# Kernel optimization log

Measured on AMD Instinct MI355X. Metric: run time of the kernel, lower is better.

Reference implementation:

```python
import jax, jax.numpy as jnp
import numpy as np

N_NODES = 100000
IN_CH = 128
HID = 16
N_EDGES = 3200000


def setup_inputs() -> dict:
    key = jax.random.key(0)
    k1, k2, k3, k4 = jax.random.split(key, 4)
    x = jax.random.normal(k1, (N_NODES, IN_CH), dtype=jnp.float32)
    edge_index = jax.random.randint(k2, (2, N_EDGES), 0, N_NODES, dtype=jnp.int64)
    s1 = 1.0 / np.sqrt(IN_CH)
    s2 = 1.0 / np.sqrt(HID)
    W1 = jax.random.uniform(k3, (IN_CH, HID), dtype=jnp.float32, minval=-s1, maxval=s1)
    b1 = jnp.zeros((HID,), dtype=jnp.float32)
    W2 = jax.random.uniform(k4, (HID, HID), dtype=jnp.float32, minval=-s2, maxval=s2)
    b2 = jnp.zeros((HID,), dtype=jnp.float32)
    return {"x": x, "edge_index": edge_index, "W1": W1, "b1": b1, "W2": W2, "b2": b2}


def _gcn_layer(h, W, b, row, col, norm, n_nodes):
    # GCNConv: transform first (small hidden dim), then normalized sum aggregation
    h = h @ W  # [N, out]
    msg = h[row] * norm[:, None]  # gather over edges incl. self-loops
    out = jax.ops.segment_sum(msg, col, num_segments=n_nodes)
    return out + b


def reference(x, edge_index, W1, b1, W2, b2):
    n = x.shape[0]
    row, col = edge_index[0], edge_index[1]
    # add self-loops (PyG GCNConv default)
    loop = jnp.arange(n, dtype=edge_index.dtype)
    row_l = jnp.concatenate([row, loop])
    col_l = jnp.concatenate([col, loop])
    # symmetric normalization D^-1/2 (A+I) D^-1/2 (degree from target index)
    deg = jax.ops.segment_sum(jnp.ones_like(col_l, dtype=x.dtype), col_l, num_segments=n)
    dinv = jnp.where(deg > 0, jax.lax.rsqrt(deg), 0.0)
    norm = dinv[row_l] * dinv[col_l]

    h = _gcn_layer(x, W1, b1, row_l, col_l, norm, n)
    h = jax.nn.relu(h)  # dropout is identity at eval
    h = _gcn_layer(h, W2, b2, row_l, col_l, norm, n)

    # fused per-edge dot-product link score + sigmoid (original edges only)
    scores = jnp.sum(h[row] * h[col], axis=-1)
    return jax.nn.sigmoid(scores)
```

## Files before the change

### kernel.cpp

```cpp
#include <hip/hip_runtime.h>
#include <hip/hip_bf16.h>
#include <hip/hip_fp16.h>
#include <math.h>


#define BSH 9
#define BSZ 512
#define MAXCH 3200
#define MAXCHUNKS 1024

__global__ __launch_bounds__(512) void pA(const int* __restrict__ col,
                                          int* __restrict__ M, int E, int CH, int NBUK) {
    __shared__ int hist[256];
    const int t = threadIdx.x, b = blockIdx.x;
    if (t < 256) hist[t] = 0;
    __syncthreads();
    const int s = b * CH, e = min(E, s + CH);
    const int n4 = (e - s) >> 2;
    const int4* c4 = (const int4*)(col + s);
    for (int i = t; i < n4; i += 512) {
        int4 c = c4[i];
        atomicAdd(&hist[c.x >> BSH], 1);
        atomicAdd(&hist[c.y >> BSH], 1);
        atomicAdd(&hist[c.z >> BSH], 1);
        atomicAdd(&hist[c.w >> BSH], 1);
    }
    for (int i = s + (n4 << 2) + t; i < e; i += 512) atomicAdd(&hist[col[i] >> BSH], 1);
    __syncthreads();
    for (int i = t; i < NBUK; i += 512) M[b * NBUK + i] = hist[i];
}

__global__ __launch_bounds__(1024) void pB1(int* __restrict__ M, int* __restrict__ T,
                                            int NBUK, int CN) {
    __shared__ int s[1024];
    const int t = threadIdx.x, k = blockIdx.x;
    int own = (t < CN) ? M[t * NBUK + k] : 0;
    s[t] = own;
    __syncthreads();
    for (int d = 1; d < 1024; d <<= 1) {
        int add = (t >= d) ? s[t - d] : 0;
        __syncthreads();
        s[t] += add;
        __syncthreads();
    }
    if (t < CN) M[t * NBUK + k] = s[t] - own;
    if (t == 1023) T[k] = s[1023];
}

__global__ __launch_bounds__(512) void pB2(const int* __restrict__ T, int* __restrict__ S,
                                           int* __restrict__ start, int NBUK, int N, int E) {
    __shared__ int s[512];
    const int t = threadIdx.x;
    int own = (t < NBUK) ? T[t] : 0;
    s[t] = own;
    __syncthreads();
    for (int d = 1; d < 512; d <<= 1) {
        int add = (t >= d) ? s[t - d] : 0;
        __syncthreads();
        s[t] += add;
        __syncthreads();
    }
    if (t < NBUK) S[t] = s[t] - own;
    if (t == 511) S[NBUK] = s[511];
    if (t == 0) start[N] = E;
}

__global__ __launch_bounds__(512) void pC(const int* __restrict__ row, const int* __restrict__ col,
                                          const int* __restrict__ M, const int* __restrict__ S,
                                          unsigned int* __restrict__ ebuf, int E, int CH, int NBUK) {
    __shared__ unsigned int se[MAXCH];
    __shared__ unsigned short pk[MAXCH];
    __shared__ int lhist[256], lbase[256], lcur[256], gbase[256];
    const int t = threadIdx.x, b = blockIdx.x;
    if (t < 256) lhist[t] = 0;
    __syncthreads();
    const int s = b * CH, e = min(E, s + CH);
    const int cnt = e - s;
    const int n4 = cnt >> 2;
    const int4* c4 = (const int4*)(col + s);
    const int4* r4 = (const int4*)(row + s);
    for (int i = t; i < n4; i += 512) {
        int4 c = c4[i];
        atomicAdd(&lhist[c.x >> BSH], 1);
        atomicAdd(&lhist[c.y >> BSH], 1);
        atomicAdd(&lhist[c.z >> BSH], 1);
        atomicAdd(&lhist[c.w >> BSH], 1);
    }
    for (int i = (n4 << 2) + t; i < cnt; i += 512) atomicAdd(&lhist[col[s + i] >> BSH], 1);
    __syncthreads();
    {
        int own = (t < 256) ? lhist[t] : 0;
        if (t < 256) lcur[t] = own;
        __syncthreads();
        for (int d = 1; d < 256; d <<= 1) {
            int add = (t < 256 && t >= d) ? lcur[t - d] : 0;
            __syncthreads();
            if (t < 256) lcur[t] += add;
            __syncthreads();
        }
        if (t < 256) {
            lbase[t] = lcur[t] - own;
            lcur[t] = lcur[t] - own;
        }
        __syncthreads();
        if (t < NBUK) gbase[t] = S[t] + M[b * NBUK + t] - lbase[t];
    }
    __syncthreads();
    for (int i = t; i < n4; i += 512) {
        int4 c = c4[i];
        int4 r = r4[i];
        int k0 = c.x >> BSH, p0 = atomicAdd(&lcur[k0], 1);
        se[p0] = ((unsigned int)(c.x & (BSZ - 1)) << 17) | (unsigned int)r.x; pk[p0] = (unsigned short)k0;
        int k1 = c.y >> BSH, p1 = atomicAdd(&lcur[k1], 1);
        se[p1] = ((unsigned int)(c.y & (BSZ - 1)) << 17) | (unsigned int)r.y; pk[p1] = (unsigned short)k1;
        int k2 = c.z >> BSH, p2 = atomicAdd(&lcur[k2], 1);
        se[p2] = ((unsigned int)(c.z & (BSZ - 1)) << 17) | (unsigned int)r.z; pk[p2] = (unsigned short)k2;
        int k3 = c.w >> BSH, p3 = atomicAdd(&lcur[k3], 1);
        se[p3] = ((unsigned int)(c.w & (BSZ - 1)) << 17) | (unsigned int)r.w; pk[p3] = (unsigned short)k3;
    }
    for (int i = (n4 << 2) + t; i < cnt; i += 512) {
        int c = col[s + i], r = row[s + i];
        int k = c >> BSH, p = atomicAdd(&lcur[k], 1);
        se[p] = ((unsigned int)(c & (BSZ - 1)) << 17) | (unsigned int)r; pk[p] = (unsigned short)k;
    }
    __syncthreads();
    for (int i = t; i < cnt; i += 512) {
        int k = pk[i];
        ebuf[gbase[k] + i] = se[i];
    }
}

__global__ __launch_bounds__(1024) void pC2(const unsigned int* __restrict__ ebuf,
                                            const int* __restrict__ S,
                                            unsigned int* __restrict__ ebuf2,
                                            float* __restrict__ dinv,
                                            int* __restrict__ start, int N) {
    __shared__ int h[BSZ], sc[BSZ], cur[BSZ];
    const int t = threadIdx.x, k = blockIdx.x;
    if (t < BSZ) h[t] = 0;
    __syncthreads();
    const int s = S[k], e = S[k + 1];
    for (int i = s + t; i < e; i += 1024) atomicAdd(&h[ebuf[i] >> 17], 1);
    __syncthreads();
    if (t < BSZ) sc[t] = h[t];
    __syncthreads();
    for (int d = 1; d < BSZ; d <<= 1) {
        int add = (t < BSZ && t >= d) ? sc[t - d] : 0;
        __syncthreads();
        if (t < BSZ) sc[t] += add;
        __syncthreads();
    }
    if (t < BSZ) {
        cur[t] = sc[t] - h[t];
        const int v = (k << BSH) + t;
        if (v < N) {
            dinv[v] = rsqrtf((float)h[t] + 1.0f);
            start[v] = s + cur[t];
        }
    }
    __syncthreads();
    for (int i = s + t; i < e; i += 1024) {
        unsigned int w = ebuf[i];
        int p = atomicAdd(&cur[w >> 17], 1);
        ebuf2[s + p] = w;
    }
}

__global__ __launch_bounds__(256) void k_gemm1(
    const float* __restrict__ x, const float* __restrict__ W1,
    const float* __restrict__ dinv, __half* __restrict__ ts, int N) {
    __shared__ float wsT[16 * 132];
    const int tid = threadIdx.x;
    for (int idx = tid; idx < 2048; idx += 256) {
        int k = idx >> 4, c = idx & 15;
        wsT[c * 132 + k] = W1[idx];
    }
    __syncthreads();
    const int n = blockIdx.x * 256 + tid;
    if (n >= N) return;
    const float4* xr = (const float4*)(x + (size_t)n * 128);
    float acc[16];
    #pragma unroll
    for (int c = 0; c < 16; ++c) acc[c] = 0.f;
    #pragma unroll 4
    for (int k4 = 0; k4 < 32; ++k4) {
        float4 a = xr[k4];
        #pragma unroll
        for (int c = 0; c < 16; ++c) {
            const float4 w = *(const float4*)&wsT[c * 132 + k4 * 4];
            acc[c] = fmaf(a.x, w.x, fmaf(a.y, w.y, fmaf(a.z, w.z, fmaf(a.w, w.w, acc[c]))));
        }
    }
    float dv = dinv[n];
    union { __half h[16]; uint4 u[2]; } o;
    #pragma unroll
    for (int c = 0; c < 16; ++c) o.h[c] = __float2half(acc[c] * dv);
    uint4* dst = (uint4*)(ts + (size_t)n * 16);
    dst[0] = o.u[0]; dst[1] = o.u[1];
}

__global__ __launch_bounds__(256) void pGat1(
    const unsigned int* __restrict__ ebuf2, const int* __restrict__ start,
    const __half2* __restrict__ tsv, const float* __restrict__ dinv,
    const float* __restrict__ b1, const float* __restrict__ W2,
    __half2* __restrict__ ts2v, int N) {
    __shared__ float w2s[256];
    const int tid = threadIdx.x;
    w2s[tid] = W2[tid];
    __syncthreads();
    const int l = tid & 7;
    const int v = blockIdx.x * 32 + (tid >> 3);
    if (v >= N) return;
    const int s = start[v], e = start[v + 1];
    float sx = 0.f, sy = 0.f;
    int i = s;
    for (; i + 8 <= e; i += 8) {
        unsigned int w0 = ebuf2[i],     w1 = ebuf2[i + 1];
        unsigned int w2 = ebuf2[i + 2], w3 = ebuf2[i + 3];
        unsigned int w4 = ebuf2[i + 4], w5 = ebuf2[i + 5];
        unsigned int w6 = ebuf2[i + 6], w7 = ebuf2[i + 7];
        float2 f0 = __half22float2(tsv[(size_t)(w0 & 0x1FFFF) * 8 + l]);
        float2 f1 = __half22float2(tsv[(size_t)(w1 & 0x1FFFF) * 8 + l]);
        float2 f2 = __half22float2(tsv[(size_t)(w2 & 0x1FFFF) * 8 + l]);
        float2 f3 = __half22float2(tsv[(size_t)(w3 & 0x1FFFF) * 8 + l]);
        float2 f4 = __half22float2(tsv[(size_t)(w4 & 0x1FFFF) * 8 + l]);
        float2 f5 = __half22float2(tsv[(size_t)(w5 & 0x1FFFF) * 8 + l]);
        float2 f6 = __half22float2(tsv[(size_t)(w6 & 0x1FFFF) * 8 + l]);
        float2 f7 = __half22float2(tsv[(size_t)(w7 & 0x1FFFF) * 8 + l]);
        sx += ((f0.x + f1.x) + (f2.x + f3.x)) + ((f4.x + f5.x) + (f6.x + f7.x));
        sy += ((f0.y + f1.y) + (f2.y + f3.y)) + ((f4.y + f5.y) + (f6.y + f7.y));
    }
    for (; i + 4 <= e; i += 4) {
        unsigned int w0 = ebuf2[i],     w1 = ebuf2[i + 1];
        unsigned int w2 = ebuf2[i + 2], w3 = ebuf2[i + 3];
        float2 f0 = __half22float2(tsv[(size_t)(w0 & 0x1FFFF) * 8 + l]);
        float2 f1 = __half22float2(tsv[(size_t)(w1 & 0x1FFFF) * 8 + l]);
        float2 f2 = __half22float2(tsv[(size_t)(w2 & 0x1FFFF) * 8 + l]);
        float2 f3 = __half22float2(tsv[(size_t)(w3 & 0x1FFFF) * 8 + l]);
        sx += (f0.x + f1.x) + (f2.x + f3.x);
        sy += (f0.y + f1.y) + (f2.y + f3.y);
    }
    for (; i < e; ++i) {
        unsigned int w = ebuf2[i];
        float2 f = __half22float2(tsv[(size_t)(w & 0x1FFFF) * 8 + l]);
        sx += f.x; sy += f.y;
    }
    const float dv = dinv[v];
    float2 sf = __half22float2(tsv[(size_t)v * 8 + l]);
    float hx = fmaxf(dv * (sx + sf.x) + b1[2 * l],     0.f);
    float hy = fmaxf(dv * (sy + sf.y) + b1[2 * l + 1], 0.f);
    float ox = 0.f, oy = 0.f;
    #pragma unroll
    for (int j = 0; j < 8; ++j) {
        float ax = __shfl(hx, j, 8);
        float ay = __shfl(hy, j, 8);
        ox = fmaf(ax, w2s[(2 * j) * 16 + 2 * l],     fmaf(ay, w2s[(2 * j + 1) * 16 + 2 * l],     ox));
        oy = fmaf(ax, w2s[(2 * j) * 16 + 2 * l + 1], fmaf(ay, w2s[(2 * j + 1) * 16 + 2 * l + 1], oy));
    }
    ts2v[(size_t)v * 8 + l] = __halves2half2(__float2half(dv * ox), __float2half(dv * oy));
}

__global__ __launch_bounds__(256) void pGat2(
    const unsigned int* __restrict__ ebuf2, const int* __restrict__ start,
    const __half2* __restrict__ tsv, const float* __restrict__ dinv,
    const float* __restrict__ b2, __half2* __restrict__ h2v, int N) {
    const int tid = threadIdx.x;
    const int l = tid & 7;
    const int v = blockIdx.x * 32 + (tid >> 3);
    if (v >= N) return;
    const int s = start[v], e = start[v + 1];
    float sx = 0.f, sy = 0.f;
    int i = s;
    for (; i + 8 <= e; i += 8) {
        unsigned int w0 = ebuf2[i],     w1 = ebuf2[i + 1];
        unsigned int w2 = ebuf2[i + 2], w3 = ebuf2[i + 3];
        unsigned int w4 = ebuf2[i + 4], w5 = ebuf2[i + 5];
        unsigned int w6 = ebuf2[i + 6], w7 = ebuf2[i + 7];
        float2 f0 = __half22float2(tsv[(size_t)(w0 & 0x1FFFF) * 8 + l]);
        float2 f1 = __half22float2(tsv[(size_t)(w1 & 0x1FFFF) * 8 + l]);
        float2 f2 = __half22float2(tsv[(size_t)(w2 & 0x1FFFF) * 8 + l]);
        float2 f3 = __half22float2(tsv[(size_t)(w3 & 0x1FFFF) * 8 + l]);
        float2 f4 = __half22float2(tsv[(size_t)(w4 & 0x1FFFF) * 8 + l]);
        float2 f5 = __half22float2(tsv[(size_t)(w5 & 0x1FFFF) * 8 + l]);
        float2 f6 = __half22float2(tsv[(size_t)(w6 & 0x1FFFF) * 8 + l]);
        float2 f7 = __half22float2(tsv[(size_t)(w7 & 0x1FFFF) * 8 + l]);
        sx += ((f0.x + f1.x) + (f2.x + f3.x)) + ((f4.x + f5.x) + (f6.x + f7.x));
        sy += ((f0.y + f1.y) + (f2.y + f3.y)) + ((f4.y + f5.y) + (f6.y + f7.y));
    }
    for (; i + 4 <= e; i += 4) {
        unsigned int w0 = ebuf2[i],     w1 = ebuf2[i + 1];
        unsigned int w2 = ebuf2[i + 2], w3 = ebuf2[i + 3];
        float2 f0 = __half22float2(tsv[(size_t)(w0 & 0x1FFFF) * 8 + l]);
        float2 f1 = __half22float2(tsv[(size_t)(w1 & 0x1FFFF) * 8 + l]);
        float2 f2 = __half22float2(tsv[(size_t)(w2 & 0x1FFFF) * 8 + l]);
        float2 f3 = __half22float2(tsv[(size_t)(w3 & 0x1FFFF) * 8 + l]);
        sx += (f0.x + f1.x) + (f2.x + f3.x);
        sy += (f0.y + f1.y) + (f2.y + f3.y);
    }
    for (; i < e; ++i) {
        unsigned int w = ebuf2[i];
        float2 f = __half22float2(tsv[(size_t)(w & 0x1FFFF) * 8 + l]);
        sx += f.x; sy += f.y;
    }
    float2 sf = __half22float2(tsv[(size_t)v * 8 + l]);
    const float dv = dinv[v];
    h2v[(size_t)v * 8 + l] = __halves2half2(
        __float2half(dv * (sx + sf.x) + b2[2 * l]),
        __float2half(dv * (sy + sf.y) + b2[2 * l + 1]));
}

__global__ void k_score(const int* __restrict__ row, const int* __restrict__ col,
                        const __half* __restrict__ h2h, float* __restrict__ out, int E) {
    int e = blockIdx.x * 256 + threadIdx.x;
    if (e < E) {
        union { uint4 u[2]; __half2 h[8]; } a, b;
        const uint4* pa = (const uint4*)(h2h + (size_t)row[e] * 16);
        const uint4* pb = (const uint4*)(h2h + (size_t)col[e] * 16);
        a.u[0] = pa[0]; a.u[1] = pa[1];
        b.u[0] = pb[0]; b.u[1] = pb[1];
        float d = 0.f;
        #pragma unroll
        for (int i = 0; i < 8; ++i) {
            float2 fa = __half22float2(a.h[i]);
            float2 fb = __half22float2(b.h[i]);
            d = fmaf(fa.x, fb.x, fmaf(fa.y, fb.y, d));
        }
        out[e] = 1.0f / (1.0f + __expf(-d));
    }
}

__global__ void k_countf(const int* __restrict__ col, float* __restrict__ deg, int E) {
    int e = blockIdx.x * 256 + threadIdx.x;
    if (e < E) atomicAdd(&deg[col[e]], 1.0f);
}
__global__ void k_dinvf(float* __restrict__ dinv, int N) {
    int v = blockIdx.x * 256 + threadIdx.x;
    if (v < N) dinv[v] = rsqrtf(dinv[v] + 1.0f);
}
__global__ __launch_bounds__(256) void k_gemm1f(
    const float* __restrict__ x, const float* __restrict__ W1,
    const float* __restrict__ dinv, float* __restrict__ ts, int N) {
    __shared__ float wsT[16 * 132];
    const int tid = threadIdx.x;
    for (int idx = tid; idx < 2048; idx += 256) {
        int k = idx >> 4, c = idx & 15;
        wsT[c * 132 + k] = W1[idx];
    }
    __syncthreads();
    const int n = blockIdx.x * 256 + tid;
    if (n >= N) return;
    const float4* xr = (const float4*)(x + (size_t)n * 128);
    float acc[16];
    #pragma unroll
    for (int c = 0; c < 16; ++c) acc[c] = 0.f;
    for (int k4 = 0; k4 < 32; ++k4) {
        float4 a = xr[k4];
        #pragma unroll
        for (int c = 0; c < 16; ++c) {
            const float4 w = *(const float4*)&wsT[c * 132 + k4 * 4];
            acc[c] = fmaf(a.x, w.x, fmaf(a.y, w.y, fmaf(a.z, w.z, fmaf(a.w, w.w, acc[c]))));
        }
    }
    float dv = dinv[n];
    float4* o = (float4*)(ts + (size_t)n * 16);
    #pragma unroll
    for (int q = 0; q < 4; ++q)
        o[q] = make_float4(acc[4*q] * dv, acc[4*q+1] * dv, acc[4*q+2] * dv, acc[4*q+3] * dv);
}
__global__ void k_scatter(const int* __restrict__ row, const int* __restrict__ col,
                          const float* __restrict__ ts, float* __restrict__ acc, int E) {
    int g = blockIdx.x * 256 + threadIdx.x;
    int e = g >> 4, c = g & 15;
    if (e < E) atomicAdd(&acc[(size_t)col[e] * 16 + c], ts[(size_t)row[e] * 16 + c]);
}
__global__ void k_finalize(float* __restrict__ acc, const float* __restrict__ ts,
                           const float* __restrict__ dinv, const float* __restrict__ b,
                           int N, int relu) {
    int g = blockIdx.x * 256 + threadIdx.x;
    int v = g >> 4, c = g & 15;
    if (v < N) {
        float h = dinv[v] * (acc[g] + ts[g]) + b[c];
        if (relu) h = fmaxf(h, 0.f);
        acc[g] = h;
    }
}
__global__ __launch_bounds__(256) void k_gemm2f(
    const float* __restrict__ h1, const float* __restrict__ W2,
    const float* __restrict__ dinv, float* __restrict__ ts2, int N) {
    __shared__ float hs[16 * 17];
    __shared__ float ws2[256];
    const int tid = threadIdx.x;
    const int base = blockIdx.x * 16;
    if (tid < 64) ((float4*)ws2)[tid] = ((const float4*)W2)[tid];
    if (tid >= 64 && tid < 128) {
        int t2 = tid - 64;
        float4 v4 = ((const float4*)(h1 + (size_t)base * 16))[t2];
        float* d = &hs[(t2 >> 2) * 17 + (t2 & 3) * 4];
        d[0] = v4.x; d[1] = v4.y; d[2] = v4.z; d[3] = v4.w;
    }
    __syncthreads();
    const int r = tid >> 4, c = tid & 15;
    float a = 0.f;
    #pragma unroll
    for (int kk = 0; kk < 16; ++kk) a = fmaf(hs[r * 17 + kk], ws2[kk * 16 + c], a);
    ts2[(size_t)(base + r) * 16 + c] = a * dinv[base + r];
}
__global__ void k_scoref(const int* __restrict__ row, const int* __restrict__ col,
                         const float* __restrict__ h2, float* __restrict__ out, int E) {
    int e = blockIdx.x * 256 + threadIdx.x;
    if (e < E) {
        const float4* a = (const float4*)(h2 + (size_t)row[e] * 16);
        const float4* b = (const float4*)(h2 + (size_t)col[e] * 16);
        float d = 0.f;
        #pragma unroll
        for (int i = 0; i < 4; ++i) {
            float4 u = a[i], v = b[i];
            d += u.x * v.x + u.y * v.y + u.z * v.z + u.w * v.w;
        }
        out[e] = 1.0f / (1.0f + __expf(-d));
    }
}

extern "C" void kernel_launch(void* const* d_in, const int* in_sizes, int n_in,
                              void* d_out, int out_size, void* d_ws, size_t ws_size,
                              hipStream_t stream) {
    const float* x  = (const float*)d_in[0];
    const int*   ei = (const int*)d_in[1];
    const float* W1 = (const float*)d_in[2];
    const float* b1 = (const float*)d_in[3];
    const float* W2 = (const float*)d_in[4];
    const float* b2 = (const float*)d_in[5];

    const int N = in_sizes[0] / 128;
    const int E = in_sizes[1] / 2;
    const int* row = ei;
    const int* col = ei + E;
    float* out = (float*)d_out;

    const int NBUK = (N + BSZ - 1) / BSZ;
    const int CN = (E + MAXCH - 1) / MAXCH;
    const int CH = MAXCH;

    char* ws = (char*)d_ws;
    size_t off = 0;
    auto alloc = [&](size_t bytes) { void* p = ws + off; off += (bytes + 255) & ~(size_t)255; return p; };
    float*  dinv  = (float*)alloc((size_t)N * 4);
    __half* ts1h  = (__half*)alloc((size_t)N * 32);
    __half* ts2h  = (__half*)alloc((size_t)N * 32);
    int*    start = (int*)alloc((size_t)(N + 1) * 4);
    int*    M     = (int*)alloc((size_t)CN * NBUK * 4);
    int*    T     = (int*)alloc((size_t)NBUK * 4);
    int*    S     = (int*)alloc((size_t)(NBUK + 1) * 4);
    unsigned int* ebuf  = (unsigned int*)alloc((size_t)E * 4);
    unsigned int* ebuf2 = (unsigned int*)alloc((size_t)E * 4);
    const size_t need = off;

    if (N <= 131072 && NBUK <= 256 && CN <= MAXCHUNKS && ws_size >= need) {
        pA <<<CN, 512, 0, stream>>>(col, M, E, CH, NBUK);
        pB1<<<NBUK, 1024, 0, stream>>>(M, T, NBUK, CN);
        pB2<<<1, 512, 0, stream>>>(T, S, start, NBUK, N, E);
        pC <<<CN, 512, 0, stream>>>(row, col, M, S, ebuf, E, CH, NBUK);
        pC2<<<NBUK, 1024, 0, stream>>>(ebuf, S, ebuf2, dinv, start, N);
        k_gemm1<<<(N + 255) / 256, 256, 0, stream>>>(x, W1, dinv, ts1h, N);
        pGat1<<<(N + 31) / 32, 256, 0, stream>>>(ebuf2, start, (const __half2*)ts1h, dinv, b1, W2,
                                                 (__half2*)ts2h, N);
        __half* h2h = ts1h;
        pGat2<<<(N + 31) / 32, 256, 0, stream>>>(ebuf2, start, (const __half2*)ts2h, dinv, b2,
                                                 (__half2*)h2h, N);
        k_score<<<(E + 255) / 256, 256, 0, stream>>>(row, col, h2h, out, E);
    } else {
        float* dinvF = (float*)ws;
        float* ts1F  = (float*)(ws + (size_t)N * 4);
        float* ts2F  = (float*)(ws + (size_t)N * 4 + (size_t)N * 64);
        hipMemsetAsync(dinvF, 0, (size_t)N * 4, stream);
        hipMemsetAsync(ts2F, 0, (size_t)N * 64, stream);
        k_countf<<<(E + 255) / 256, 256, 0, stream>>>(col, dinvF, E);
        k_dinvf<<<(N + 255) / 256, 256, 0, stream>>>(dinvF, N);
        k_gemm1f<<<(N + 255) / 256, 256, 0, stream>>>(x, W1, dinvF, ts1F, N);
        k_scatter<<<(E * 16) / 256, 256, 0, stream>>>(row, col, ts1F, ts2F, E);
        k_finalize<<<(N * 16 + 255) / 256, 256, 0, stream>>>(ts2F, ts1F, dinvF, b1, N, 1);
        k_gemm2f<<<N / 16, 256, 0, stream>>>(ts2F, W2, dinvF, ts1F, N);
        hipMemsetAsync(ts2F, 0, (size_t)N * 64, stream);
        k_scatter<<<(E * 16) / 256, 256, 0, stream>>>(row, col, ts1F, ts2F, E);
        k_finalize<<<(N * 16 + 255) / 256, 256, 0, stream>>>(ts2F, ts1F, dinvF, b2, N, 0);
        k_scoref<<<(E + 255) / 256, 256, 0, stream>>>(row, col, ts2F, out, E);
    }
}
```

Before: 253.9 us.

## Fuse per-bucket local sort into gather kernels and compute degrees via global atomics

Shrinks destination buckets to 128 nodes and drops the separate pC2 second-level sort pass and its ebuf2 buffer. Each gather kernel now re-sorts its bucket's edges in shared memory before aggregating, and falls back to a slow scan when a bucket exceeds capacity. Degrees are counted with global atomics in pA, and dinv is computed inside gemm1. This removes one full pass over the edge list and a buffer, but the local sort is done twice and pA now issues millions of global atomics.

```diff
diff --git a/kernel.cpp b/kernel.cpp
--- a/kernel.cpp
+++ b/kernel.cpp
@@ -4,28 +4,34 @@
 #include <math.h>
 
 
-#define BSH 9
-#define BSZ 512
+#define BSH 7
+#define BSZ 128
+#define CAP 8192
 #define MAXCH 3200
 #define MAXCHUNKS 1024
 
 __global__ __launch_bounds__(512) void pA(const int* __restrict__ col,
-                                          int* __restrict__ M, int E, int CH, int NBUK) {
-    __shared__ int hist[256];
+                                          int* __restrict__ M, int* __restrict__ degi,
+                                          int E, int CH, int NBUK) {
+    __shared__ int hist[1024];
     const int t = threadIdx.x, b = blockIdx.x;
-    if (t < 256) hist[t] = 0;
+    for (int i = t; i < 1024; i += 512) hist[i] = 0;
     __syncthreads();
     const int s = b * CH, e = min(E, s + CH);
     const int n4 = (e - s) >> 2;
     const int4* c4 = (const int4*)(col + s);
     for (int i = t; i < n4; i += 512) {
         int4 c = c4[i];
-        atomicAdd(&hist[c.x >> BSH], 1);
-        atomicAdd(&hist[c.y >> BSH], 1);
-        atomicAdd(&hist[c.z >> BSH], 1);
-        atomicAdd(&hist[c.w >> BSH], 1);
-    }
-    for (int i = s + (n4 << 2) + t; i < e; i += 512) atomicAdd(&hist[col[i] >> BSH], 1);
+        atomicAdd(&hist[c.x >> BSH], 1); atomicAdd(&degi[c.x], 1);
+        atomicAdd(&hist[c.y >> BSH], 1); atomicAdd(&degi[c.y], 1);
+        atomicAdd(&hist[c.z >> BSH], 1); atomicAdd(&degi[c.z], 1);
+        atomicAdd(&hist[c.w >> BSH], 1); atomicAdd(&degi[c.w], 1);
+    }
+    for (int i = s + (n4 << 2) + t; i < e; i += 512) {
+        int c = col[i];
+        atomicAdd(&hist[c >> BSH], 1);
+        atomicAdd(&degi[c], 1);
+    }
     __syncthreads();
     for (int i = t; i < NBUK; i += 512) M[b * NBUK + i] = hist[i];
 }
@@ -47,66 +53,63 @@
     if (t == 1023) T[k] = s[1023];
 }
 
-__global__ __launch_bounds__(512) void pB2(const int* __restrict__ T, int* __restrict__ S,
-                                           int* __restrict__ start, int NBUK, int N, int E) {
-    __shared__ int s[512];
+__global__ __launch_bounds__(1024) void pB2(const int* __restrict__ T, int* __restrict__ S,
+                                            int NBUK) {
+    __shared__ int s[1024];
     const int t = threadIdx.x;
     int own = (t < NBUK) ? T[t] : 0;
     s[t] = own;
     __syncthreads();
-    for (int d = 1; d < 512; d <<= 1) {
+    for (int d = 1; d < 1024; d <<= 1) {
         int add = (t >= d) ? s[t - d] : 0;
         __syncthreads();
         s[t] += add;
         __syncthreads();
     }
     if (t < NBUK) S[t] = s[t] - own;
-    if (t == 511) S[NBUK] = s[511];
-    if (t == 0) start[N] = E;
-}
-
-__global__ __launch_bounds__(512) void pC(const int* __restrict__ row, const int* __restrict__ col,
-                                          const int* __restrict__ M, const int* __restrict__ S,
-                                          unsigned int* __restrict__ ebuf, int E, int CH, int NBUK) {
+    if (t == 1023) S[NBUK] = s[1023];
+}
+
+__global__ __launch_bounds__(1024) void pC(const int* __restrict__ row, const int* __restrict__ col,
+                                           const int* __restrict__ M, const int* __restrict__ S,
+                                           unsigned int* __restrict__ ebuf, int E, int CH, int NBUK) {
     __shared__ unsigned int se[MAXCH];
     __shared__ unsigned short pk[MAXCH];
-    __shared__ int lhist[256], lbase[256], lcur[256], gbase[256];
+    __shared__ int lhist[1024], lbase[1024], lcur[1024], gbase[1024];
     const int t = threadIdx.x, b = blockIdx.x;
-    if (t < 256) lhist[t] = 0;
+    lhist[t] = 0;
     __syncthreads();
     const int s = b * CH, e = min(E, s + CH);
     const int cnt = e - s;
     const int n4 = cnt >> 2;
     const int4* c4 = (const int4*)(col + s);
     const int4* r4 = (const int4*)(row + s);
-    for (int i = t; i < n4; i += 512) {
+    for (int i = t; i < n4; i += 1024) {
         int4 c = c4[i];
         atomicAdd(&lhist[c.x >> BSH], 1);
         atomicAdd(&lhist[c.y >> BSH], 1);
         atomicAdd(&lhist[c.z >> BSH], 1);
         atomicAdd(&lhist[c.w >> BSH], 1);
     }
-    for (int i = (n4 << 2) + t; i < cnt; i += 512) atomicAdd(&lhist[col[s + i] >> BSH], 1);
+    for (int i = (n4 << 2) + t; i < cnt; i += 1024) atomicAdd(&lhist[col[s + i] >> BSH], 1);
     __syncthreads();
     {
-        int own = (t < 256) ? lhist[t] : 0;
-        if (t < 256) lcur[t] = own;
-        __syncthreads();
-        for (int d = 1; d < 256; d <<= 1) {
-            int add = (t < 256 && t >= d) ? lcur[t - d] : 0;
+        int own = lhist[t];
+        lcur[t] = own;
+        __syncthreads();
+        for (int d = 1; d < 1024; d <<= 1) {
+            int add = (t >= d) ? lcur[t - d] : 0;
             __syncthreads();
-            if (t < 256) lcur[t] += add;
+            lcur[t] += add;
             __syncthreads();
         }
-        if (t < 256) {
-            lbase[t] = lcur[t] - own;
-            lcur[t] = lcur[t] - own;
-        }
+        lbase[t] = lcur[t] - own;
+        lcur[t] = lbase[t];
         __syncthreads();
         if (t < NBUK) gbase[t] = S[t] + M[b * NBUK + t] - lbase[t];
     }
     __syncthreads();
-    for (int i = t; i < n4; i += 512) {
+    for (int i = t; i < n4; i += 1024) {
         int4 c = c4[i];
         int4 r = r4[i];
         int k0 = c.x >> BSH, p0 = atomicAdd(&lcur[k0], 1);
@@ -118,57 +121,22 @@
         int k3 = c.w >> BSH, p3 = atomicAdd(&lcur[k3], 1);
         se[p3] = ((unsigned int)(c.w & (BSZ - 1)) << 17) | (unsigned int)r.w; pk[p3] = (unsigned short)k3;
     }
-    for (int i = (n4 << 2) + t; i < cnt; i += 512) {
+    for (int i = (n4 << 2) + t; i < cnt; i += 1024) {
         int c = col[s + i], r = row[s + i];
         int k = c >> BSH, p = atomicAdd(&lcur[k], 1);
         se[p] = ((unsigned int)(c & (BSZ - 1)) << 17) | (unsigned int)r; pk[p] = (unsigned short)k;
     }
     __syncthreads();
-    for (int i = t; i < cnt; i += 512) {
+    for (int i = t; i < cnt; i += 1024) {
         int k = pk[i];
         ebuf[gbase[k] + i] = se[i];
     }
 }
 
-__global__ __launch_bounds__(1024) void pC2(const unsigned int* __restrict__ ebuf,
-                                            const int* __restrict__ S,
-                                            unsigned int* __restrict__ ebuf2,
-                                            float* __restrict__ dinv,
-                                            int* __restrict__ start, int N) {
-    __shared__ int h[BSZ], sc[BSZ], cur[BSZ];
-    const int t = threadIdx.x, k = blockIdx.x;
-    if (t < BSZ) h[t] = 0;
-    __syncthreads();
-    const int s = S[k], e = S[k + 1];
-    for (int i = s + t; i < e; i += 1024) atomicAdd(&h[ebuf[i] >> 17], 1);
-    __syncthreads();
-    if (t < BSZ) sc[t] = h[t];
-    __syncthreads();
-    for (int d = 1; d < BSZ; d <<= 1) {
-        int add = (t < BSZ && t >= d) ? sc[t - d] : 0;
-        __syncthreads();
-        if (t < BSZ) sc[t] += add;
-        __syncthreads();
-    }
-    if (t < BSZ) {
-        cur[t] = sc[t] - h[t];
-        const int v = (k << BSH) + t;
-        if (v < N) {
-            dinv[v] = rsqrtf((float)h[t] + 1.0f);
-            start[v] = s + cur[t];
-        }
-    }
-    __syncthreads();
-    for (int i = s + t; i < e; i += 1024) {
-        unsigned int w = ebuf[i];
-        int p = atomicAdd(&cur[w >> 17], 1);
-        ebuf2[s + p] = w;
-    }
-}
-
 __global__ __launch_bounds__(256) void k_gemm1(
     const float* __restrict__ x, const float* __restrict__ W1,
-    const float* __restrict__ dinv, __half* __restrict__ ts, int N) {
+    const int* __restrict__ degi, float* __restrict__ dinv,
+    __half* __restrict__ ts, int N) {
     __shared__ float wsT[16 * 132];
     const int tid = threadIdx.x;
     for (int idx = tid; idx < 2048; idx += 256) {
@@ -191,7 +159,8 @@
             acc[c] = fmaf(a.x, w.x, fmaf(a.y, w.y, fmaf(a.z, w.z, fmaf(a.w, w.w, acc[c]))));
         }
     }
-    float dv = dinv[n];
+    const float dv = rsqrtf((float)degi[n] + 1.0f);
+    dinv[n] = dv;
     union { __half h[16]; uint4 u[2]; } o;
     #pragma unroll
     for (int c = 0; c < 16; ++c) o.h[c] = __float2half(acc[c] * dv);
@@ -199,114 +168,159 @@
     dst[0] = o.u[0]; dst[1] = o.u[1];
 }
 
-__global__ __launch_bounds__(256) void pGat1(
-    const unsigned int* __restrict__ ebuf2, const int* __restrict__ start,
+__global__ __launch_bounds__(512) void pG1(
+    const unsigned int* __restrict__ ebuf, const int* __restrict__ S,
     const __half2* __restrict__ tsv, const float* __restrict__ dinv,
     const float* __restrict__ b1, const float* __restrict__ W2,
     __half2* __restrict__ ts2v, int N) {
+    __shared__ unsigned int se[CAP];
+    __shared__ int h[BSZ], sc[BSZ], cur[BSZ];
     __shared__ float w2s[256];
-    const int tid = threadIdx.x;
-    w2s[tid] = W2[tid];
-    __syncthreads();
-    const int l = tid & 7;
-    const int v = blockIdx.x * 32 + (tid >> 3);
-    if (v >= N) return;
-    const int s = start[v], e = start[v + 1];
-    float sx = 0.f, sy = 0.f;
-    int i = s;
-    for (; i + 8 <= e; i += 8) {
-        unsigned int w0 = ebuf2[i],     w1 = ebuf2[i + 1];
-        unsigned int w2 = ebuf2[i + 2], w3 = ebuf2[i + 3];
-        unsigned int w4 = ebuf2[i + 4], w5 = ebuf2[i + 5];
-        unsigned int w6 = ebuf2[i + 6], w7 = ebuf2[i + 7];
-        float2 f0 = __half22float2(tsv[(size_t)(w0 & 0x1FFFF) * 8 + l]);
-        float2 f1 = __half22float2(tsv[(size_t)(w1 & 0x1FFFF) * 8 + l]);
-        float2 f2 = __half22float2(tsv[(size_t)(w2 & 0x1FFFF) * 8 + l]);
-        float2 f3 = __half22float2(tsv[(size_t)(w3 & 0x1FFFF) * 8 + l]);
-        float2 f4 = __half22float2(tsv[(size_t)(w4 & 0x1FFFF) * 8 + l]);
-        float2 f5 = __half22float2(tsv[(size_t)(w5 & 0x1FFFF) * 8 + l]);
-        float2 f6 = __half22float2(tsv[(size_t)(w6 & 0x1FFFF) * 8 + l]);
-        float2 f7 = __half22float2(tsv[(size_t)(w7 & 0x1FFFF) * 8 + l]);
-        sx += ((f0.x + f1.x) + (f2.x + f3.x)) + ((f4.x + f5.x) + (f6.x + f7.x));
-        sy += ((f0.y + f1.y) + (f2.y + f3.y)) + ((f4.y + f5.y) + (f6.y + f7.y));
-    }
-    for (; i + 4 <= e; i += 4) {
-        unsigned int w0 = ebuf2[i],     w1 = ebuf2[i + 1];
-        unsigned int w2 = ebuf2[i + 2], w3 = ebuf2[i + 3];
-        float2 f0 = __half22float2(tsv[(size_t)(w0 & 0x1FFFF) * 8 + l]);
-        float2 f1 = __half22float2(tsv[(size_t)(w1 & 0x1FFFF) * 8 + l]);
-        float2 f2 = __half22float2(tsv[(size_t)(w2 & 0x1FFFF) * 8 + l]);
-        float2 f3 = __half22float2(tsv[(size_t)(w3 & 0x1FFFF) * 8 + l]);
-        sx += (f0.x + f1.x) + (f2.x + f3.x);
-        sy += (f0.y + f1.y) + (f2.y + f3.y);
-    }
-    for (; i < e; ++i) {
-        unsigned int w = ebuf2[i];
-        float2 f = __half22float2(tsv[(size_t)(w & 0x1FFFF) * 8 + l]);
-        sx += f.x; sy += f.y;
-    }
-    const float dv = dinv[v];
-    float2 sf = __half22float2(tsv[(size_t)v * 8 + l]);
-    float hx = fmaxf(dv * (sx + sf.x) + b1[2 * l],     0.f);
-    float hy = fmaxf(dv * (sy + sf.y) + b1[2 * l + 1], 0.f);
-    float ox = 0.f, oy = 0.f;
-    #pragma unroll
-    for (int j = 0; j < 8; ++j) {
-        float ax = __shfl(hx, j, 8);
-        float ay = __shfl(hy, j, 8);
-        ox = fmaf(ax, w2s[(2 * j) * 16 + 2 * l],     fmaf(ay, w2s[(2 * j + 1) * 16 + 2 * l],     ox));
-        oy = fmaf(ax, w2s[(2 * j) * 16 + 2 * l + 1], fmaf(ay, w2s[(2 * j + 1) * 16 + 2 * l + 1], oy));
-    }
-    ts2v[(size_t)v * 8 + l] = __halves2half2(__float2half(dv * ox), __float2half(dv * oy));
-}
-
-__global__ __launch_bounds__(256) void pGat2(
-    const unsigned int* __restrict__ ebuf2, const int* __restrict__ start,
+    const int t = threadIdx.x, k = blockIdx.x;
+    if (t < BSZ) h[t] = 0;
+    if (t < 256) w2s[t] = W2[t];
+    __syncthreads();
+    const int s = S[k], e = S[k + 1];
+    const int cnt = e - s;
+    if (cnt <= CAP) {
+        for (int i = s + t; i < e; i += 512) atomicAdd(&h[ebuf[i] >> 17], 1);
+        __syncthreads();
+        if (t < BSZ) sc[t] = h[t];
+        __syncthreads();
+        for (int d = 1; d < BSZ; d <<= 1) {
+            int add = (t < BSZ && t >= d) ? sc[t - d] : 0;
+            __syncthreads();
+            if (t < BSZ) sc[t] += add;
+            __syncthreads();
+        }
+        if (t < BSZ) cur[t] = sc[t] - h[t];
+        __syncthreads();
+        for (int i = s + t; i < e; i += 512) {
+            unsigned int w = ebuf[i];
+            int p = atomicAdd(&cur[w >> 17], 1);
+            se[p] = w;
+        }
+        __syncthreads();
+    }
+    const int l = t & 7;
+    #pragma unroll
+    for (int sweep = 0; sweep < 2; ++sweep) {
+        const int lv = (t >> 3) + (sweep << 6);
+        const int v = (k << BSH) + lv;
+        if (v >= N) continue;
+        float sx = 0.f, sy = 0.f;
+        if (cnt <= CAP) {
+            const int pe = sc[lv];
+            int i = pe - h[lv];
+            for (; i + 4 <= pe; i += 4) {
+                unsigned int w0 = se[i], w1 = se[i + 1], w2 = se[i + 2], w3 = se[i + 3];
+                float2 f0 = __half22float2(tsv[(size_t)(w0 & 0x1FFFF) * 8 + l]);
+                float2 f1 = __half22float2(tsv[(size_t)(w1 & 0x1FFFF) * 8 + l]);
+                float2 f2 = __half22float2(tsv[(size_t)(w2 & 0x1FFFF) * 8 + l]);
+                float2 f3 = __half22float2(tsv[(size_t)(w3 & 0x1FFFF) * 8 + l]);
+                sx += (f0.x + f1.x) + (f2.x + f3.x);
+                sy += (f0.y + f1.y) + (f2.y + f3.y);
+            }
+            for (; i < pe; ++i) {
+                unsigned int w = se[i];
+                float2 f = __half22float2(tsv[(size_t)(w & 0x1FFFF) * 8 + l]);
+                sx += f.x; sy += f.y;
+            }
+        } else {
+            for (int j = s; j < e; ++j) {
+                unsigned int w = ebuf[j];
+                if ((int)(w >> 17) == lv) {
+                    float2 f = __half22float2(tsv[(size_t)(w & 0x1FFFF) * 8 + l]);
+                    sx += f.x; sy += f.y;
+                }
+            }
+        }
+        const float dv = dinv[v];
+        float2 sf = __half22float2(tsv[(size_t)v * 8 + l]);
+        float hx = fmaxf(dv * (sx + sf.x) + b1[2 * l],     0.f);
+        float hy = fmaxf(dv * (sy + sf.y) + b1[2 * l + 1], 0.f);
+        float ox = 0.f, oy = 0.f;
+        #pragma unroll
+        for (int j = 0; j < 8; ++j) {
+            float ax = __shfl(hx, j, 8);
+            float ay = __shfl(hy, j, 8);
+            ox = fmaf(ax, w2s[(2 * j) * 16 + 2 * l],     fmaf(ay, w2s[(2 * j + 1) * 16 + 2 * l],     ox));
+            oy = fmaf(ax, w2s[(2 * j) * 16 + 2 * l + 1], fmaf(ay, w2s[(2 * j + 1) * 16 + 2 * l + 1], oy));
+        }
+        ts2v[(size_t)v * 8 + l] = __halves2half2(__float2half(dv * ox), __float2half(dv * oy));
+    }
+}
+
+__global__ __launch_bounds__(512) void pG2(
+    const unsigned int* __restrict__ ebuf, const int* __restrict__ S,
     const __half2* __restrict__ tsv, const float* __restrict__ dinv,
     const float* __restrict__ b2, __half2* __restrict__ h2v, int N) {
-    const int tid = threadIdx.x;
-    const int l = tid & 7;
-    const int v = blockIdx.x * 32 + (tid >> 3);
-    if (v >= N) return;
-    const int s = start[v], e = start[v + 1];
-    float sx = 0.f, sy = 0.f;
-    int i = s;
-    for (; i + 8 <= e; i += 8) {
-        unsigned int w0 = ebuf2[i],     w1 = ebuf2[i + 1];
-        unsigned int w2 = ebuf2[i + 2], w3 = ebuf2[i + 3];
-        unsigned int w4 = ebuf2[i + 4], w5 = ebuf2[i + 5];
-        unsigned int w6 = ebuf2[i + 6], w7 = ebuf2[i + 7];
-        float2 f0 = __half22float2(tsv[(size_t)(w0 & 0x1FFFF) * 8 + l]);
-        float2 f1 = __half22float2(tsv[(size_t)(w1 & 0x1FFFF) * 8 + l]);
-        float2 f2 = __half22float2(tsv[(size_t)(w2 & 0x1FFFF) * 8 + l]);
-        float2 f3 = __half22float2(tsv[(size_t)(w3 & 0x1FFFF) * 8 + l]);
-        float2 f4 = __half22float2(tsv[(size_t)(w4 & 0x1FFFF) * 8 + l]);
-        float2 f5 = __half22float2(tsv[(size_t)(w5 & 0x1FFFF) * 8 + l]);
-        float2 f6 = __half22float2(tsv[(size_t)(w6 & 0x1FFFF) * 8 + l]);
-        float2 f7 = __half22float2(tsv[(size_t)(w7 & 0x1FFFF) * 8 + l]);
-        sx += ((f0.x + f1.x) + (f2.x + f3.x)) + ((f4.x + f5.x) + (f6.x + f7.x));
-        sy += ((f0.y + f1.y) + (f2.y + f3.y)) + ((f4.y + f5.y) + (f6.y + f7.y));
-    }
-    for (; i + 4 <= e; i += 4) {
-        unsigned int w0 = ebuf2[i],     w1 = ebuf2[i + 1];
-        unsigned int w2 = ebuf2[i + 2], w3 = ebuf2[i + 3];
-        float2 f0 = __half22float2(tsv[(size_t)(w0 & 0x1FFFF) * 8 + l]);
-        float2 f1 = __half22float2(tsv[(size_t)(w1 & 0x1FFFF) * 8 + l]);
-        float2 f2 = __half22float2(tsv[(size_t)(w2 & 0x1FFFF) * 8 + l]);
-        float2 f3 = __half22float2(tsv[(size_t)(w3 & 0x1FFFF) * 8 + l]);
-        sx += (f0.x + f1.x) + (f2.x + f3.x);
-        sy += (f0.y + f1.y) + (f2.y + f3.y);
-    }
-    for (; i < e; ++i) {
-        unsigned int w = ebuf2[i];
-        float2 f = __half22float2(tsv[(size_t)(w & 0x1FFFF) * 8 + l]);
-        sx += f.x; sy += f.y;
-    }
-    float2 sf = __half22float2(tsv[(size_t)v * 8 + l]);
-    const float dv = dinv[v];
-    h2v[(size_t)v * 8 + l] = __halves2half2(
-        __float2half(dv * (sx + sf.x) + b2[2 * l]),
-        __float2half(dv * (sy + sf.y) + b2[2 * l + 1]));
+    __shared__ unsigned int se[CAP];
+    __shared__ int h[BSZ], sc[BSZ], cur[BSZ];
+    const int t = threadIdx.x, k = blockIdx.x;
+    if (t < BSZ) h[t] = 0;
+    __syncthreads();
+    const int s = S[k], e = S[k + 1];
+    const int cnt = e - s;
+    if (cnt <= CAP) {
+        for (int i = s + t; i < e; i += 512) atomicAdd(&h[ebuf[i] >> 17], 1);
+        __syncthreads();
+        if (t < BSZ) sc[t] = h[t];
+        __syncthreads();
+        for (int d = 1; d < BSZ; d <<= 1) {
+            int add = (t < BSZ && t >= d) ? sc[t - d] : 0;
+            __syncthreads();
+            if (t < BSZ) sc[t] += add;
+            __syncthreads();
+        }
+        if (t < BSZ) cur[t] = sc[t] - h[t];
+        __syncthreads();
+        for (int i = s + t; i < e; i += 512) {
+            unsigned int w = ebuf[i];
+            int p = atomicAdd(&cur[w >> 17], 1);
+            se[p] = w;
+        }
+        __syncthreads();
+    }
+    const int l = t & 7;
+    #pragma unroll
+    for (int sweep = 0; sweep < 2; ++sweep) {
+        const int lv = (t >> 3) + (sweep << 6);
+        const int v = (k << BSH) + lv;
+        if (v >= N) continue;
+        float sx = 0.f, sy = 0.f;
+        if (cnt <= CAP) {
+            const int pe = sc[lv];
+            int i = pe - h[lv];
+            for (; i + 4 <= pe; i += 4) {
+                unsigned int w0 = se[i], w1 = se[i + 1], w2 = se[i + 2], w3 = se[i + 3];
+                float2 f0 = __half22float2(tsv[(size_t)(w0 & 0x1FFFF) * 8 + l]);
+                float2 f1 = __half22float2(tsv[(size_t)(w1 & 0x1FFFF) * 8 + l]);
+                float2 f2 = __half22float2(tsv[(size_t)(w2 & 0x1FFFF) * 8 + l]);
+                float2 f3 = __half22float2(tsv[(size_t)(w3 & 0x1FFFF) * 8 + l]);
+                sx += (f0.x + f1.x) + (f2.x + f3.x);
+                sy += (f0.y + f1.y) + (f2.y + f3.y);
+            }
+            for (; i < pe; ++i) {
+                unsigned int w = se[i];
+                float2 f = __half22float2(tsv[(size_t)(w & 0x1FFFF) * 8 + l]);
+                sx += f.x; sy += f.y;
+            }
+        } else {
+            for (int j = s; j < e; ++j) {
+                unsigned int w = ebuf[j];
+                if ((int)(w >> 17) == lv) {
+                    float2 f = __half22float2(tsv[(size_t)(w & 0x1FFFF) * 8 + l]);
+                    sx += f.x; sy += f.y;
+                }
+            }
+        }
+        float2 sf = __half22float2(tsv[(size_t)v * 8 + l]);
+        const float dv = dinv[v];
+        h2v[(size_t)v * 8 + l] = __halves2half2(
+            __float2half(dv * (sx + sf.x) + b2[2 * l]),
+            __float2half(dv * (sy + sf.y) + b2[2 * l + 1]));
+    }
 }
 
 __global__ void k_score(const int* __restrict__ row, const int* __restrict__ col,
@@ -447,26 +461,25 @@
     float*  dinv  = (float*)alloc((size_t)N * 4);
     __half* ts1h  = (__half*)alloc((size_t)N * 32);
     __half* ts2h  = (__half*)alloc((size_t)N * 32);
-    int*    start = (int*)alloc((size_t)(N + 1) * 4);
+    int*    degi  = (int*)alloc((size_t)N * 4);
     int*    M     = (int*)alloc((size_t)CN * NBUK * 4);
     int*    T     = (int*)alloc((size_t)NBUK * 4);
     int*    S     = (int*)alloc((size_t)(NBUK + 1) * 4);
     unsigned int* ebuf  = (unsigned int*)alloc((size_t)E * 4);
-    unsigned int* ebuf2 = (unsigned int*)alloc((size_t)E * 4);
     const size_t need = off;
 
-    if (N <= 131072 && NBUK <= 256 && CN <= MAXCHUNKS && ws_size >= need) {
-        pA <<<CN, 512, 0, stream>>>(col, M, E, CH, NBUK);
+    if (N <= 131072 && NBUK <= 1024 && CN <= MAXCHUNKS && ws_size >= need) {
+        hipMemsetAsync(degi, 0, (size_t)N * 4, stream);
+        pA <<<CN, 512, 0, stream>>>(col, M, degi, E, CH, NBUK);
         pB1<<<NBUK, 1024, 0, stream>>>(M, T, NBUK, CN);
-        pB2<<<1, 512, 0, stream>>>(T, S, start, NBUK, N, E);
-        pC <<<CN, 512, 0, stream>>>(row, col, M, S, ebuf, E, CH, NBUK);
-        pC2<<<NBUK, 1024, 0, stream>>>(ebuf, S, ebuf2, dinv, start, N);
-        k_gemm1<<<(N + 255) / 256, 256, 0, stream>>>(x, W1, dinv, ts1h, N);
-        pGat1<<<(N + 31) / 32, 256, 0, stream>>>(ebuf2, start, (const __half2*)ts1h, dinv, b1, W2,
-                                                 (__half2*)ts2h, N);
+        pB2<<<1, 1024, 0, stream>>>(T, S, NBUK);
+        k_gemm1<<<(N + 255) / 256, 256, 0, stream>>>(x, W1, degi, dinv, ts1h, N);
+        pC <<<CN, 1024, 0, stream>>>(row, col, M, S, ebuf, E, CH, NBUK);
+        pG1<<<NBUK, 512, 0, stream>>>(ebuf, S, (const __half2*)ts1h, dinv, b1, W2,
+                                      (__half2*)ts2h, N);
         __half* h2h = ts1h;
-        pGat2<<<(N + 31) / 32, 256, 0, stream>>>(ebuf2, start, (const __half2*)ts2h, dinv, b2,
-                                                 (__half2*)h2h, N);
+        pG2<<<NBUK, 512, 0, stream>>>(ebuf, S, (const __half2*)ts2h, dinv, b2,
+                                      (__half2*)h2h, N);
         k_score<<<(E + 255) / 256, 256, 0, stream>>>(row, col, h2h, out, E);
     } else {
         float* dinvF = (float*)ws;
```

After: 382.1 us. 50.5% more time.

## Replace histogram prefix-scan bucketing with atomic fixed-capacity bucket allocation

Applied to the files above, without the earlier changes.

Drops the separate histogram pass and the two prefix-scan kernels. The sort kernel now reserves space in each bucket with a global atomicAdd into fixed-capacity (CAPB) bucket slots, and the downstream kernels take bucket extents from the per-bucket counters. This cuts the column index read and two kernel launches from the preprocessing phase. In exchange it relies on no bucket overflowing CAPB, which is only guarded by a loose total-size check, and it makes edge order within a bucket nondeterministic.

```diff
diff --git a/kernel.cpp b/kernel.cpp
--- a/kernel.cpp
+++ b/kernel.cpp
@@ -6,68 +6,14 @@
 
 #define BSH 9
 #define BSZ 512
+#define CAPB 32768
 #define MAXCH 3200
 #define MAXCHUNKS 1024
 
-__global__ __launch_bounds__(512) void pA(const int* __restrict__ col,
-                                          int* __restrict__ M, int E, int CH, int NBUK) {
-    __shared__ int hist[256];
-    const int t = threadIdx.x, b = blockIdx.x;
-    if (t < 256) hist[t] = 0;
-    __syncthreads();
-    const int s = b * CH, e = min(E, s + CH);
-    const int n4 = (e - s) >> 2;
-    const int4* c4 = (const int4*)(col + s);
-    for (int i = t; i < n4; i += 512) {
-        int4 c = c4[i];
-        atomicAdd(&hist[c.x >> BSH], 1);
-        atomicAdd(&hist[c.y >> BSH], 1);
-        atomicAdd(&hist[c.z >> BSH], 1);
-        atomicAdd(&hist[c.w >> BSH], 1);
-    }
-    for (int i = s + (n4 << 2) + t; i < e; i += 512) atomicAdd(&hist[col[i] >> BSH], 1);
-    __syncthreads();
-    for (int i = t; i < NBUK; i += 512) M[b * NBUK + i] = hist[i];
-}
-
-__global__ __launch_bounds__(1024) void pB1(int* __restrict__ M, int* __restrict__ T,
-                                            int NBUK, int CN) {
-    __shared__ int s[1024];
-    const int t = threadIdx.x, k = blockIdx.x;
-    int own = (t < CN) ? M[t * NBUK + k] : 0;
-    s[t] = own;
-    __syncthreads();
-    for (int d = 1; d < 1024; d <<= 1) {
-        int add = (t >= d) ? s[t - d] : 0;
-        __syncthreads();
-        s[t] += add;
-        __syncthreads();
-    }
-    if (t < CN) M[t * NBUK + k] = s[t] - own;
-    if (t == 1023) T[k] = s[1023];
-}
-
-__global__ __launch_bounds__(512) void pB2(const int* __restrict__ T, int* __restrict__ S,
-                                           int* __restrict__ start, int NBUK, int N, int E) {
-    __shared__ int s[512];
-    const int t = threadIdx.x;
-    int own = (t < NBUK) ? T[t] : 0;
-    s[t] = own;
-    __syncthreads();
-    for (int d = 1; d < 512; d <<= 1) {
-        int add = (t >= d) ? s[t - d] : 0;
-        __syncthreads();
-        s[t] += add;
-        __syncthreads();
-    }
-    if (t < NBUK) S[t] = s[t] - own;
-    if (t == 511) S[NBUK] = s[511];
-    if (t == 0) start[N] = E;
-}
-
-__global__ __launch_bounds__(512) void pC(const int* __restrict__ row, const int* __restrict__ col,
-                                          const int* __restrict__ M, const int* __restrict__ S,
-                                          unsigned int* __restrict__ ebuf, int E, int CH, int NBUK) {
+__global__ __launch_bounds__(512) void pSort(
+    const int* __restrict__ row, const int* __restrict__ col,
+    int* __restrict__ gcur, unsigned int* __restrict__ ebuf,
+    int E, int CH, int NBUK) {
     __shared__ unsigned int se[MAXCH];
     __shared__ unsigned short pk[MAXCH];
     __shared__ int lhist[256], lbase[256], lcur[256], gbase[256];
@@ -103,7 +49,10 @@
             lcur[t] = lcur[t] - own;
         }
         __syncthreads();
-        if (t < NBUK) gbase[t] = S[t] + M[b * NBUK + t] - lbase[t];
+        if (t < NBUK) {
+            int base = atomicAdd(&gcur[t], lhist[t]);
+            gbase[t] = t * CAPB + base - lbase[t];
+        }
     }
     __syncthreads();
     for (int i = t; i < n4; i += 512) {
@@ -130,8 +79,8 @@
     }
 }
 
-__global__ __launch_bounds__(1024) void pC2(const unsigned int* __restrict__ ebuf,
-                                            const int* __restrict__ S,
+__global__ __launch_bounds__(1024) void pS2(const unsigned int* __restrict__ ebuf,
+                                            const int* __restrict__ gcur,
                                             unsigned int* __restrict__ ebuf2,
                                             float* __restrict__ dinv,
                                             int* __restrict__ start, int N) {
@@ -139,7 +88,7 @@
     const int t = threadIdx.x, k = blockIdx.x;
     if (t < BSZ) h[t] = 0;
     __syncthreads();
-    const int s = S[k], e = S[k + 1];
+    const int s = k * CAPB, e = s + gcur[k];
     for (int i = s + t; i < e; i += 1024) atomicAdd(&h[ebuf[i] >> 17], 1);
     __syncthreads();
     if (t < BSZ) sc[t] = h[t];
@@ -201,6 +150,7 @@
 
 __global__ __launch_bounds__(256) void pGat1(
     const unsigned int* __restrict__ ebuf2, const int* __restrict__ start,
+    const int* __restrict__ gcur,
     const __half2* __restrict__ tsv, const float* __restrict__ dinv,
     const float* __restrict__ b1, const float* __restrict__ W2,
     __half2* __restrict__ ts2v, int N) {
@@ -211,7 +161,10 @@
     const int l = tid & 7;
     const int v = blockIdx.x * 32 + (tid >> 3);
     if (v >= N) return;
-    const int s = start[v], e = start[v + 1];
+    const int s = start[v];
+    const int k = v >> BSH;
+    const bool lastv = (((v + 1) & (BSZ - 1)) == 0) || (v + 1 >= N);
+    const int e = lastv ? (k * CAPB + gcur[k]) : start[v + 1];
     float sx = 0.f, sy = 0.f;
     int i = s;
     for (; i + 8 <= e; i += 8) {
@@ -262,13 +215,17 @@
 
 __global__ __launch_bounds__(256) void pGat2(
     const unsigned int* __restrict__ ebuf2, const int* __restrict__ start,
+    const int* __restrict__ gcur,
     const __half2* __restrict__ tsv, const float* __restrict__ dinv,
     const float* __restrict__ b2, __half2* __restrict__ h2v, int N) {
     const int tid = threadIdx.x;
     const int l = tid & 7;
     const int v = blockIdx.x * 32 + (tid >> 3);
     if (v >= N) return;
-    const int s = start[v], e = start[v + 1];
+    const int s = start[v];
+    const int k = v >> BSH;
+    const bool lastv = (((v + 1) & (BSZ - 1)) == 0) || (v + 1 >= N);
+    const int e = lastv ? (k * CAPB + gcur[k]) : start[v + 1];
     float sx = 0.f, sy = 0.f;
     int i = s;
     for (; i + 8 <= e; i += 8) {
@@ -448,25 +405,22 @@
     __half* ts1h  = (__half*)alloc((size_t)N * 32);
     __half* ts2h  = (__half*)alloc((size_t)N * 32);
     int*    start = (int*)alloc((size_t)(N + 1) * 4);
-    int*    M     = (int*)alloc((size_t)CN * NBUK * 4);
-    int*    T     = (int*)alloc((size_t)NBUK * 4);
-    int*    S     = (int*)alloc((size_t)(NBUK + 1) * 4);
-    unsigned int* ebuf  = (unsigned int*)alloc((size_t)E * 4);
-    unsigned int* ebuf2 = (unsigned int*)alloc((size_t)E * 4);
+    int*    gcur  = (int*)alloc((size_t)NBUK * 4);
+    unsigned int* ebuf  = (unsigned int*)alloc((size_t)NBUK * CAPB * 4);
+    unsigned int* ebuf2 = (unsigned int*)alloc((size_t)NBUK * CAPB * 4);
     const size_t need = off;
 
-    if (N <= 131072 && NBUK <= 256 && CN <= MAXCHUNKS && ws_size >= need) {
-        pA <<<CN, 512, 0, stream>>>(col, M, E, CH, NBUK);
-        pB1<<<NBUK, 1024, 0, stream>>>(M, T, NBUK, CN);
-        pB2<<<1, 512, 0, stream>>>(T, S, start, NBUK, N, E);
-        pC <<<CN, 512, 0, stream>>>(row, col, M, S, ebuf, E, CH, NBUK);
-        pC2<<<NBUK, 1024, 0, stream>>>(ebuf, S, ebuf2, dinv, start, N);
+    if (N <= 131072 && NBUK <= 256 && CN <= MAXCHUNKS &&
+        (size_t)E * 2 <= (size_t)NBUK * CAPB && ws_size >= need) {
+        hipMemsetAsync(gcur, 0, (size_t)NBUK * 4, stream);
+        pSort<<<CN, 512, 0, stream>>>(row, col, gcur, ebuf, E, CH, NBUK);
+        pS2<<<NBUK, 1024, 0, stream>>>(ebuf, gcur, ebuf2, dinv, start, N);
         k_gemm1<<<(N + 255) / 256, 256, 0, stream>>>(x, W1, dinv, ts1h, N);
-        pGat1<<<(N + 31) / 32, 256, 0, stream>>>(ebuf2, start, (const __half2*)ts1h, dinv, b1, W2,
-                                                 (__half2*)ts2h, N);
+        pGat1<<<(N + 31) / 32, 256, 0, stream>>>(ebuf2, start, gcur, (const __half2*)ts1h,
+                                                 dinv, b1, W2, (__half2*)ts2h, N);
         __half* h2h = ts1h;
-        pGat2<<<(N + 31) / 32, 256, 0, stream>>>(ebuf2, start, (const __half2*)ts2h, dinv, b2,
-                                                 (__half2*)h2h, N);
+        pGat2<<<(N + 31) / 32, 256, 0, stream>>>(ebuf2, start, gcur, (const __half2*)ts2h,
+                                                 dinv, b2, (__half2*)h2h, N);
         k_score<<<(E + 255) / 256, 256, 0, stream>>>(row, col, h2h, out, E);
     } else {
         float* dinvF = (float*)ws;
```

Result: no change. 257.6 us (+1.5%).
